# Optimization experiments

Measured on AMD Instinct MI355X. Metric: run time of the kernel, lower is better.

Reference implementation:

```python
import jax, jax.numpy as jnp
import numpy as np

E = 8        # num_experts
K = 2        # num_experts_per_tok
H = 1024     # hidden_dim
F = 2816     # intermediate_dim
R = 256      # shared-core rank
B, S = 2, 1024


def setup_inputs() -> dict:
    key = jax.random.key(0)
    ks = jax.random.split(key, 12)
    inp = {
        "hidden_states": jax.random.normal(ks[0], (B, S, H), jnp.float32),
        "gate_w": jax.random.normal(ks[1], (H, E), jnp.float32) / np.sqrt(H),
        # gate_proj: hidden -> intermediate, factored W_e = Ug[e] @ Cg @ Vg[e]
        "Ug": jax.random.normal(ks[2], (E, H, R), jnp.float32) / np.sqrt(H),
        "Cg": jax.random.normal(ks[3], (R, R), jnp.float32) / np.sqrt(R),
        "Vg": jax.random.normal(ks[4], (E, R, F), jnp.float32) / np.sqrt(R),
        # up_proj: hidden -> intermediate
        "Uu": jax.random.normal(ks[5], (E, H, R), jnp.float32) / np.sqrt(H),
        "Cu": jax.random.normal(ks[6], (R, R), jnp.float32) / np.sqrt(R),
        "Vu": jax.random.normal(ks[7], (E, R, F), jnp.float32) / np.sqrt(R),
        # down_proj: intermediate -> hidden
        "Ud": jax.random.normal(ks[8], (E, F, R), jnp.float32) / np.sqrt(F),
        "Cd": jax.random.normal(ks[9], (R, R), jnp.float32) / np.sqrt(R),
        "Vd": jax.random.normal(ks[10], (E, R, H), jnp.float32) / np.sqrt(R),
    }
    return inp


def _moe_forward(x, gate_w, Ug, Cg, Vg, Uu, Cu, Vu, Ud, Cd, Vd):
    b, s, h = x.shape
    xf = x.reshape(-1, h)                       # [T, H]
    T = xf.shape[0]
    logits = xf @ gate_w                        # [T, E]
    probs = jax.nn.softmax(logits, axis=-1)
    w, idx = jax.lax.top_k(probs, K)            # [T, K]
    w = w / jnp.sum(w, axis=-1, keepdims=True)
    # dense combine weights: combine[t, e] = sum of renormalized routing
    # weights over top-k slots routed to expert e (scatter-add in torch code)
    combine = jnp.zeros((T, E), xf.dtype).at[jnp.arange(T)[:, None], idx].add(w)
    out = jnp.zeros_like(xf)
    for e in range(E):  # fixed small expert count
        g = (xf @ Ug[e]) @ Cg @ Vg[e]           # [T, F]
        u = (xf @ Uu[e]) @ Cu @ Vu[e]           # [T, F]
        a = jax.nn.silu(g) * u
        y = (a @ Ud[e]) @ Cd @ Vd[e]            # [T, H]
        out = out + combine[:, e:e + 1] * y
    return out.reshape(b, s, h)


def reference(hidden_states, gate_w, Ug, Cg, Vg, Uu, Cu, Vu, Ud, Cd, Vd):
    return _moe_forward(hidden_states, gate_w, Ug, Cg, Vg, Uu, Cu, Vu, Ud, Cd, Vd)
```

## Files before the change

kernel.cpp:

```cpp
#include <hip/hip_runtime.h>
#include <math.h>

constexpr int cE = 8;
constexpr int cH = 1024;
constexpr int cF = 2816;
constexpr int cR = 256;
constexpr int cT = 2048;
constexpr int ROWS = cT * 2;
constexpr int LDA = 40;

using short8  = __attribute__((ext_vector_type(8))) short;
using float4v = __attribute__((ext_vector_type(4))) float;
#define MFMA16 __builtin_amdgcn_mfma_f32_16x16x32_bf16

__device__ __forceinline__ unsigned short f2bf(float f) {
  union { float f; unsigned u; } v; v.f = f;
  unsigned r = v.u + 0x7fffu + ((v.u >> 16) & 1u);
  return (unsigned short)(r >> 16);
}
__device__ __forceinline__ float bf2f(unsigned short s) {
  union { unsigned u; float f; } v; v.u = (unsigned)s << 16; return v.f;
}

__device__ __forceinline__ void store_bf8(unsigned short* dst, float4 a, float4 b) {
  union { unsigned short u[8]; uint4 v; } t;
  t.u[0] = f2bf(a.x); t.u[1] = f2bf(a.y); t.u[2] = f2bf(a.z); t.u[3] = f2bf(a.w);
  t.u[4] = f2bf(b.x); t.u[5] = f2bf(b.y); t.u[6] = f2bf(b.z); t.u[7] = f2bf(b.w);
  *reinterpret_cast<uint4*>(dst) = t.v;
}

__device__ __forceinline__ void gld16(const unsigned short* g, unsigned short* l) {
  __builtin_amdgcn_global_load_lds(
      (const __attribute__((address_space(1))) void*)g,
      (__attribute__((address_space(3))) void*)l, 16, 0, 0);
}

__device__ __forceinline__ void tconv_tile64(
    const float* __restrict__ in, unsigned short* __restrict__ out,
    int P, int Q, int e, int bx, int by, int tid, float (*tile)[65])
{
  const long es = (long)P * Q;
  in += e * es; out += e * es;
  const int c0 = bx * 64, r0 = by * 64;
  const int r = tid >> 4, c4 = (tid & 15) * 4;
#pragma unroll
  for (int p = 0; p < 4; ++p) {
    float4 v = *reinterpret_cast<const float4*>(
        in + (long)(r0 + p * 16 + r) * Q + c0 + c4);
    tile[p * 16 + r][c4 + 0] = v.x; tile[p * 16 + r][c4 + 1] = v.y;
    tile[p * 16 + r][c4 + 2] = v.z; tile[p * 16 + r][c4 + 3] = v.w;
  }
  __syncthreads();
  const int cc = tid >> 4, rr4 = (tid & 15) * 4;
#pragma unroll
  for (int p = 0; p < 4; ++p) {
    ushort4 o;
    o.x = f2bf(tile[rr4 + 0][p * 16 + cc]);
    o.y = f2bf(tile[rr4 + 1][p * 16 + cc]);
    o.z = f2bf(tile[rr4 + 2][p * 16 + cc]);
    o.w = f2bf(tile[rr4 + 3][p * 16 + cc]);
    *reinterpret_cast<ushort4*>(out + (long)(c0 + p * 16 + cc) * P + r0 + rr4) = o;
  }
}

constexpr int P1_TCONV = 544;
constexpr int PREP1_BLOCKS = P1_TCONV + cT / 4;

__global__ __launch_bounds__(256) void k_prep1s(
    const float* __restrict__ Cg, unsigned short* __restrict__ CgT,
    const float* __restrict__ Cu, unsigned short* __restrict__ CuT,
    const float* __restrict__ Vd, unsigned short* __restrict__ VdT,
    const float* __restrict__ x, const float* __restrict__ gw,
    unsigned short* __restrict__ xb, int* __restrict__ et,
    float* __restrict__ wt)
{
  __shared__ float tile[64][65];
  int b = blockIdx.x;
  const int tid = threadIdx.x;
  if (b < P1_TCONV) {
    const float* in; unsigned short* out; int P, Q;
    if (b < 16)       { in = Cg; out = CgT; P = 256; Q = 256;  }
    else if (b < 32)  { b -= 16; in = Cu; out = CuT; P = 256; Q = 256;  }
    else              { b -= 32; in = Vd; out = VdT; P = 256; Q = 1024; }
    const int tpe = (P / 64) * (Q / 64);
    const int e = b / tpe, rem = b % tpe;
    const int bx = rem % (Q / 64), by = rem / (Q / 64);
    tconv_tile64(in, out, P, Q, e, bx, by, tid, tile);
    return;
  }
  const int wid = tid >> 6, lane = tid & 63;
  const int t = (b - P1_TCONV) * 4 + wid;
  const float* xr = x + (long)t * cH + lane * 16;
  float4 v0 = *reinterpret_cast<const float4*>(xr);
  float4 v1 = *reinterpret_cast<const float4*>(xr + 4);
  float4 v2 = *reinterpret_cast<const float4*>(xr + 8);
  float4 v3 = *reinterpret_cast<const float4*>(xr + 12);
  store_bf8(xb + (long)t * cH + lane * 16, v0, v1);
  store_bf8(xb + (long)t * cH + lane * 16 + 8, v2, v3);
  float xv[16];
  *reinterpret_cast<float4*>(&xv[0])  = v0;
  *reinterpret_cast<float4*>(&xv[4])  = v1;
  *reinterpret_cast<float4*>(&xv[8])  = v2;
  *reinterpret_cast<float4*>(&xv[12]) = v3;
  const float* g = gw + (long)lane * 16 * cE;
  float l[cE];
#pragma unroll
  for (int e = 0; e < cE; ++e) l[e] = 0.f;
#pragma unroll
  for (int i = 0; i < 16; ++i) {
    float4 ga = *reinterpret_cast<const float4*>(g + i * cE);
    float4 gb = *reinterpret_cast<const float4*>(g + i * cE + 4);
    float xi = xv[i];
    l[0] += xi * ga.x; l[1] += xi * ga.y; l[2] += xi * ga.z; l[3] += xi * ga.w;
    l[4] += xi * gb.x; l[5] += xi * gb.y; l[6] += xi * gb.z; l[7] += xi * gb.w;
  }
#pragma unroll
  for (int m = 1; m < 64; m <<= 1)
#pragma unroll
    for (int e = 0; e < cE; ++e)
      l[e] += __shfl_xor(l[e], m, 64);
  if (lane == 0) {
    int i0 = 0; float m0 = l[0];
#pragma unroll
    for (int e = 1; e < cE; ++e) if (l[e] > m0) { m0 = l[e]; i0 = e; }
    int i1 = -1; float m1 = -1e30f;
#pragma unroll
    for (int e = 0; e < cE; ++e) if (e != i0 && l[e] > m1) { m1 = l[e]; i1 = e; }
    float w0 = 1.f / (1.f + expf(m1 - m0));
    et[t * 2 + 0] = i0;  et[t * 2 + 1] = i1;
    wt[t * 2 + 0] = w0;  wt[t * 2 + 1] = 1.f - w0;
  }
}

__device__ __forceinline__ void foldm_body(
    const unsigned short* __restrict__ A, const float* __restrict__ B,
    unsigned short* __restrict__ D, int ldd, int m0, int n0, int tid,
    unsigned short* As, unsigned short* Bs)
{
  const int sr = tid >> 2, sk = (tid & 3) * 8;
  const unsigned short* a0 = A + (long)(m0 + sr) * 256 + sk;
  const unsigned short* a1 = a0 + (long)64 * 256;
  const float* br = B + (long)(n0 + sr) * 256 + sk;
  uint4 rA0, rA1; float4 rB0, rB1;
  auto load_slice = [&](int k0) {
    rA0 = *reinterpret_cast<const uint4*>(a0 + k0);
    rA1 = *reinterpret_cast<const uint4*>(a1 + k0);
    rB0 = *reinterpret_cast<const float4*>(br + k0);
    rB1 = *reinterpret_cast<const float4*>(br + k0 + 4);
  };
  load_slice(0);
  const int wid = tid >> 6, lane = tid & 63;
  const int wm = (wid >> 1) * 64, wn = (wid & 1) * 32;
  const int fr = lane & 15, fq = lane >> 4;
  float4v zf = {0.f, 0.f, 0.f, 0.f};
  float4v acc[4][2];
#pragma unroll
  for (int i = 0; i < 4; ++i) { acc[i][0] = zf; acc[i][1] = zf; }
  for (int k0 = 0; k0 < 256; k0 += 32) {
    *reinterpret_cast<uint4*>(&As[sr * LDA + sk]) = rA0;
    *reinterpret_cast<uint4*>(&As[(sr + 64) * LDA + sk]) = rA1;
    store_bf8(&Bs[sr * LDA + sk], rB0, rB1);
    if (k0 + 32 < 256) load_slice(k0 + 32);
    __syncthreads();
    short8 af[4], bf[2];
#pragma unroll
    for (int mi = 0; mi < 4; ++mi)
      af[mi] = *reinterpret_cast<const short8*>(&As[(wm + mi * 16 + fr) * LDA + fq * 8]);
#pragma unroll
    for (int nj = 0; nj < 2; ++nj)
      bf[nj] = *reinterpret_cast<const short8*>(&Bs[(wn + nj * 16 + fr) * LDA + fq * 8]);
#pragma unroll
    for (int mi = 0; mi < 4; ++mi)
#pragma unroll
      for (int nj = 0; nj < 2; ++nj)
        acc[mi][nj] = MFMA16(af[mi], bf[nj], acc[mi][nj], 0, 0, 0);
    __syncthreads();
  }
#pragma unroll
  for (int mi = 0; mi < 4; ++mi)
#pragma unroll
    for (int r = 0; r < 4; ++r) {
      int m = m0 + wm + mi * 16 + fq * 4 + r;
#pragma unroll
      for (int nj = 0; nj < 2; ++nj)
        D[(long)m * ldd + n0 + wn + nj * 16 + fr] = f2bf(acc[mi][nj][r]);
    }
}

constexpr int PREP2_BLOCKS = 769 + 3 * 1408;
__global__ __launch_bounds__(256, 3) void k_prep2(
    const unsigned short* __restrict__ CgT, const unsigned short* __restrict__ CuT,
    const float* __restrict__ Ug, const float* __restrict__ Uu,
    unsigned short* __restrict__ b1t,
    const unsigned short* __restrict__ VdT, const float* __restrict__ Cd,
    unsigned short* __restrict__ vd2t,
    const float* __restrict__ Vg, unsigned short* __restrict__ vgT,
    const float* __restrict__ Vu, unsigned short* __restrict__ vuT,
    const float* __restrict__ Ud, unsigned short* __restrict__ udT,
    const int* __restrict__ et, int* __restrict__ rowmap,
    int* __restrict__ tok, int* __restrict__ cnt, int* __restrict__ off)
{
  __shared__ __align__(16) char smem[64 * 65 * 4];
  const int b = blockIdx.x;
  const int tid = threadIdx.x;
  if (b < 512) {
    unsigned short* As = (unsigned short*)smem;
    unsigned short* Bs = As + 128 * LDA;
    const int bx = b & 15, by = (b >> 4) & 1, z = b >> 5;
    const int sel = z >> 3, e = z & 7;
    const unsigned short* A = sel ? CuT : CgT;
    const float* B = (sel ? Uu : Ug) + (long)e * cH * cR;
    unsigned short* Dp = b1t + (long)e * 512 * 1024 + (long)sel * 256 * 1024;
    foldm_body(A, B, Dp, cH, by * 128, bx * 64, tid, As, Bs);
  } else if (b < 768) {
    unsigned short* As = (unsigned short*)smem;
    unsigned short* Bs = As + 128 * LDA;
    const int b2 = b - 512;
    const int bx = b2 & 3, by = (b2 >> 2) & 7, e = b2 >> 5;
    foldm_body(VdT + (long)e * cH * cR, Cd, vd2t + (long)e * cH * 256, cR,
               by * 128, bx * 64, tid, As, Bs);
  } else if (b == 768) {
    int* sc_ = (int*)smem;
    int* sp_ = sc_ + cE;
    int* so_ = sc_ + 2 * cE;
    if (tid < cE) { sc_[tid] = 0; sp_[tid] = 0; }
    __syncthreads();
    for (int i = tid; i < ROWS; i += 256) atomicAdd(&sc_[et[i]], 1);
    __syncthreads();
    if (tid == 0) {
      int s = 0;
      for (int e = 0; e < cE; ++e) { so_[e] = s; s += sc_[e]; }
    }
    __syncthreads();
    for (int i = tid; i < ROWS; i += 256) {
      int e = et[i];
      int slot = atomicAdd(&sp_[e], 1);
      int cr = so_[e] + slot;
      rowmap[i] = cr;
      tok[cr] = i >> 1;
    }
    if (tid < cE) { cnt[tid] = sc_[tid]; off[tid] = so_[tid]; }
  } else {
    float (*tile)[65] = reinterpret_cast<float(*)[65]>(smem);
    int t = b - 769;
    const float* in; unsigned short* out; int P, Q;
    if (t < 1408)       { in = Vg; out = vgT; P = 256;  Q = 2816; }
    else if (t < 2816)  { t -= 1408; in = Vu; out = vuT; P = 256;  Q = 2816; }
    else                { t -= 2816; in = Ud; out = udT; P = 2816; Q = 256;  }
    const int tpe = (P / 64) * (Q / 64);
    const int e = t / tpe, rem = t % tpe;
    const int bx = rem % (Q / 64), by = rem / (Q / 64);
    tconv_tile64(in, out, P, Q, e, bx, by, tid, tile);
  }
}

__global__ __launch_bounds__(256, 4) void k_t1c(
    const unsigned short* __restrict__ xb, const unsigned short* __restrict__ b1t,
    unsigned short* __restrict__ t1, const int* __restrict__ tok,
    const int* __restrict__ cnt, const int* __restrict__ off)
{
  __shared__ __align__(16) unsigned short As[2][64 * 64], Bs[2][64 * 64];
  const int e = blockIdx.z, c = cnt[e], o = off[e];
  const int m0 = blockIdx.y * 64;
  if (m0 >= c) return;
  const int n0 = blockIdx.x * 64;
  const int tid = threadIdx.x;
  const int wid = tid >> 6, lane = tid & 63;
  const int sr8 = lane >> 3;
  const int scs = ((lane & 7) ^ sr8) * 8;
  const unsigned short* gA[2];
#pragma unroll
  for (int j = 0; j < 2; ++j) {
    int row = min(m0 + wid * 16 + j * 8 + sr8, c - 1);
    gA[j] = xb + (long)tok[o + row] * cH + scs;
  }
  const unsigned short* gB = b1t + (long)e * 512 * 1024 +
      (long)(n0 + wid * 16 + sr8) * 1024 + scs;
  const int lofs = wid * 16 * 64;
  auto STAGE = [&](int k0, int buf) {
    gld16(gA[0] + k0, &As[buf][lofs]);
    gld16(gA[1] + k0, &As[buf][lofs + 8 * 64]);
    gld16(gB + k0, &Bs[buf][lofs]);
    gld16(gB + (long)8 * 1024 + k0, &Bs[buf][lofs + 8 * 64]);
  };
  const int wm = (wid >> 1) * 32, wn = (wid & 1) * 32;
  const int fr = lane & 15, fq = lane >> 4;
  const int swz = (fr & 7) * 8;
  float4v zf = {0.f, 0.f, 0.f, 0.f};
  float4v acc[2][2] = {{zf, zf}, {zf, zf}};
  STAGE(0, 0);
  __syncthreads();
  for (int t = 0; t < 16; ++t) {
    const int cur = t & 1;
    if (t < 15) STAGE((t + 1) * 64, cur ^ 1);
#pragma unroll
    for (int ks = 0; ks < 2; ++ks) {
      short8 af[2], bf[2];
#pragma unroll
      for (int mi = 0; mi < 2; ++mi)
        af[mi] = *reinterpret_cast<const short8*>(
            &As[cur][(wm + mi * 16 + fr) * 64 + ((ks * 32 + fq * 8) ^ swz)]);
#pragma unroll
      for (int nj = 0; nj < 2; ++nj)
        bf[nj] = *reinterpret_cast<const short8*>(
            &Bs[cur][(wn + nj * 16 + fr) * 64 + ((ks * 32 + fq * 8) ^ swz)]);
#pragma unroll
      for (int mi = 0; mi < 2; ++mi)
#pragma unroll
        for (int nj = 0; nj < 2; ++nj)
          acc[mi][nj] = MFMA16(af[mi], bf[nj], acc[mi][nj], 0, 0, 0);
    }
    __syncthreads();
  }
#pragma unroll
  for (int mi = 0; mi < 2; ++mi)
#pragma unroll
    for (int r = 0; r < 4; ++r) {
      int row = m0 + wm + mi * 16 + fq * 4 + r;
      if (row < c) {
#pragma unroll
        for (int nj = 0; nj < 2; ++nj)
          t1[(long)(o + row) * 512 + n0 + wn + nj * 16 + fr] = f2bf(acc[mi][nj][r]);
      }
    }
}

__global__ __launch_bounds__(256, 4) void k_act(
    const unsigned short* __restrict__ t1,
    const unsigned short* __restrict__ vgT, const unsigned short* __restrict__ vuT,
    unsigned short* __restrict__ a, const int* __restrict__ cnt,
    const int* __restrict__ off)
{
  __shared__ __align__(16) unsigned short Ag[2][64 * 32], Au[2][64 * 32];
  __shared__ __align__(16) unsigned short Bg[2][64 * 32], Bu[2][64 * 32];
  const int e = blockIdx.z, c = cnt[e], o = off[e];
  const int m0 = blockIdx.y * 64;
  if (m0 >= c) return;
  const int n0 = blockIdx.x * 64;
  const int tid = threadIdx.x;
  const int wid = tid >> 6, lane = tid & 63;
  const int sr16 = lane >> 2;
  const int scs = (((lane & 3) ^ (sr16 & 3)) * 8);
  const int ra = o + min(m0 + wid * 16 + sr16, c - 1);
  const unsigned short* gAg = t1 + (long)ra * 512 + scs;
  const unsigned short* gBg = vgT + (long)e * cF * 256 + (long)(n0 + wid * 16 + sr16) * 256 + scs;
  const unsigned short* gBu = vuT + (long)e * cF * 256 + (long)(n0 + wid * 16 + sr16) * 256 + scs;
  const int lofs = wid * 16 * 32;
  auto STAGE = [&](int k0, int buf) {
    gld16(gAg + k0, &Ag[buf][lofs]);
    gld16(gAg + 256 + k0, &Au[buf][lofs]);
    gld16(gBg + k0, &Bg[buf][lofs]);
    gld16(gBu + k0, &Bu[buf][lofs]);
  };
  const int wm = (wid >> 1) * 32, wn = (wid & 1) * 32;
  const int fr = lane & 15, fq = lane >> 4;
  const int swz = (fr & 3) * 8;
  float4v zf = {0.f, 0.f, 0.f, 0.f};
  float4v accg[2][2] = {{zf, zf}, {zf, zf}};
  float4v accu[2][2] = {{zf, zf}, {zf, zf}};
  STAGE(0, 0);
  __syncthreads();
  for (int t = 0; t < 8; ++t) {
    const int cur = t & 1;
    if (t < 7) STAGE((t + 1) * 32, cur ^ 1);
    short8 ag[2], au[2], bg[2], bu[2];
#pragma unroll
    for (int mi = 0; mi < 2; ++mi) {
      ag[mi] = *reinterpret_cast<const short8*>(
          &Ag[cur][(wm + mi * 16 + fr) * 32 + ((fq * 8) ^ swz)]);
      au[mi] = *reinterpret_cast<const short8*>(
          &Au[cur][(wm + mi * 16 + fr) * 32 + ((fq * 8) ^ swz)]);
    }
#pragma unroll
    for (int nj = 0; nj < 2; ++nj) {
      bg[nj] = *reinterpret_cast<const short8*>(
          &Bg[cur][(wn + nj * 16 + fr) * 32 + ((fq * 8) ^ swz)]);
      bu[nj] = *reinterpret_cast<const short8*>(
          &Bu[cur][(wn + nj * 16 + fr) * 32 + ((fq * 8) ^ swz)]);
    }
#pragma unroll
    for (int mi = 0; mi < 2; ++mi)
#pragma unroll
      for (int nj = 0; nj < 2; ++nj) {
        accg[mi][nj] = MFMA16(ag[mi], bg[nj], accg[mi][nj], 0, 0, 0);
        accu[mi][nj] = MFMA16(au[mi], bu[nj], accu[mi][nj], 0, 0, 0);
      }
    __syncthreads();
  }
#pragma unroll
  for (int mi = 0; mi < 2; ++mi)
#pragma unroll
    for (int r = 0; r < 4; ++r) {
      int row = m0 + wm + mi * 16 + fq * 4 + r;
      if (row < c) {
#pragma unroll
        for (int nj = 0; nj < 2; ++nj) {
          float g = accg[mi][nj][r];
          float u = accu[mi][nj][r];
          float s = g / (1.f + expf(-g)) * u;
          a[(long)(o + row) * cF + n0 + wn + nj * 16 + fr] = f2bf(s);
        }
      }
    }
}

__global__ __launch_bounds__(256, 4) void k_t3(
    const unsigned short* __restrict__ a, const unsigned short* __restrict__ udT,
    float* __restrict__ t3p, const int* __restrict__ cnt,
    const int* __restrict__ off)
{
  __shared__ __align__(16) unsigned short As[2][64 * 64], Bs[2][64 * 64];
  const int e = blockIdx.z, c = cnt[e], o = off[e];
  const int m0 = blockIdx.y * 64;
  if (m0 >= c) return;
  const int n0 = (blockIdx.x & 3) * 64;
  const int ksp = blockIdx.x >> 2;
  const int kbase = ksp * 704;
  const int tid = threadIdx.x;
  const int wid = tid >> 6, lane = tid & 63;
  const int sr8 = lane >> 3;
  const int scs = ((lane & 7) ^ sr8) * 8;
  const int ra0 = o + min(m0 + wid * 16 + sr8, c - 1);
  const int ra1 = o + min(m0 + wid * 16 + 8 + sr8, c - 1);
  const unsigned short* gA0 = a + (long)ra0 * cF + kbase + scs;
  const unsigned short* gA1 = a + (long)ra1 * cF + kbase + scs;
  const unsigned short* gB  = udT + (long)e * 256 * cF +
      (long)(n0 + wid * 16 + sr8) * cF + kbase + scs;
  const int lofs = wid * 16 * 64;
  auto STAGE = [&](int k0, int buf) {
    gld16(gA0 + k0, &As[buf][lofs]);
    gld16(gA1 + k0, &As[buf][lofs + 8 * 64]);
    gld16(gB + k0, &Bs[buf][lofs]);
    gld16(gB + (long)8 * cF + k0, &Bs[buf][lofs + 8 * 64]);
  };
  const int wm = (wid >> 1) * 32, wn = (wid & 1) * 32;
  const int fr = lane & 15, fq = lane >> 4;
  const int swz = (fr & 7) * 8;
  float4v zf = {0.f, 0.f, 0.f, 0.f};
  float4v acc[2][2] = {{zf, zf}, {zf, zf}};
  STAGE(0, 0);
  __syncthreads();
  for (int t = 0; t < 11; ++t) {
    const int cur = t & 1;
    if (t < 10) STAGE((t + 1) * 64, cur ^ 1);
#pragma unroll
    for (int ks = 0; ks < 2; ++ks) {
      short8 af[2], bf[2];
#pragma unroll
      for (int mi = 0; mi < 2; ++mi)
        af[mi] = *reinterpret_cast<const short8*>(
            &As[cur][(wm + mi * 16 + fr) * 64 + ((ks * 32 + fq * 8) ^ swz)]);
#pragma unroll
      for (int nj = 0; nj < 2; ++nj)
        bf[nj] = *reinterpret_cast<const short8*>(
            &Bs[cur][(wn + nj * 16 + fr) * 64 + ((ks * 32 + fq * 8) ^ swz)]);
#pragma unroll
      for (int mi = 0; mi < 2; ++mi)
#pragma unroll
        for (int nj = 0; nj < 2; ++nj)
          acc[mi][nj] = MFMA16(af[mi], bf[nj], acc[mi][nj], 0, 0, 0);
    }
    __syncthreads();
  }
  float* dstbase = t3p + (long)ksp * ROWS * 256;
#pragma unroll
  for (int mi = 0; mi < 2; ++mi)
#pragma unroll
    for (int r = 0; r < 4; ++r) {
      int row = m0 + wm + mi * 16 + fq * 4 + r;
      if (row < c) {
        float* dst = dstbase + (long)(o + row) * 256 + n0 + wn;
#pragma unroll
        for (int nj = 0; nj < 2; ++nj)
          dst[nj * 16 + fr] = acc[mi][nj][r];
      }
    }
}

__global__ __launch_bounds__(256) void k_red(
    const float* __restrict__ t3p, unsigned short* __restrict__ t3b)
{
  const long psz = (long)ROWS * 256;
  long i = ((long)blockIdx.x * 256 + threadIdx.x) * 8;
  float4 s0 = *reinterpret_cast<const float4*>(t3p + i);
  float4 s1 = *reinterpret_cast<const float4*>(t3p + i + 4);
#pragma unroll
  for (int q = 1; q < 4; ++q) {
    float4 a0 = *reinterpret_cast<const float4*>(t3p + q * psz + i);
    float4 a1 = *reinterpret_cast<const float4*>(t3p + q * psz + i + 4);
    s0.x += a0.x; s0.y += a0.y; s0.z += a0.z; s0.w += a0.w;
    s1.x += a1.x; s1.y += a1.y; s1.z += a1.z; s1.w += a1.w;
  }
  store_bf8(t3b + i, s0, s1);
}

__global__ __launch_bounds__(256, 4) void k_y(
    const unsigned short* __restrict__ t3b, const unsigned short* __restrict__ vd2t,
    unsigned short* __restrict__ y, const int* __restrict__ cnt,
    const int* __restrict__ off)
{
  __shared__ __align__(16) unsigned short As[2][64 * 32], Bs[2][64 * 32];
  const int e = blockIdx.z, c = cnt[e], o = off[e];
  const int m0 = blockIdx.y * 64;
  if (m0 >= c) return;
  const int n0 = blockIdx.x * 64;
  const int tid = threadIdx.x;
  const int wid = tid >> 6, lane = tid & 63;
  const int sr16 = lane >> 2;
  const int scs = (((lane & 3) ^ (sr16 & 3)) * 8);
  const int ra = o + min(m0 + wid * 16 + sr16, c - 1);
  const unsigned short* gA = t3b + (long)ra * 256 + scs;
  const unsigned short* gB = vd2t + (long)e * cH * 256 + (long)(n0 + wid * 16 + sr16) * 256 + scs;
  const int lofs = wid * 16 * 32;
  auto STAGE = [&](int k0, int buf) {
    gld16(gA + k0, &As[buf][lofs]);
    gld16(gB + k0, &Bs[buf][lofs]);
  };
  const int wm = (wid >> 1) * 32, wn = (wid & 1) * 32;
  const int fr = lane & 15, fq = lane >> 4;
  const int swz = (fr & 3) * 8;
  float4v zf = {0.f, 0.f, 0.f, 0.f};
  float4v acc[2][2] = {{zf, zf}, {zf, zf}};
  STAGE(0, 0);
  __syncthreads();
  for (int t = 0; t < 8; ++t) {
    const int cur = t & 1;
    if (t < 7) STAGE((t + 1) * 32, cur ^ 1);
    short8 af[2], bf[2];
#pragma unroll
    for (int mi = 0; mi < 2; ++mi)
      af[mi] = *reinterpret_cast<const short8*>(
          &As[cur][(wm + mi * 16 + fr) * 32 + ((fq * 8) ^ swz)]);
#pragma unroll
    for (int nj = 0; nj < 2; ++nj)
      bf[nj] = *reinterpret_cast<const short8*>(
          &Bs[cur][(wn + nj * 16 + fr) * 32 + ((fq * 8) ^ swz)]);
#pragma unroll
    for (int mi = 0; mi < 2; ++mi)
#pragma unroll
      for (int nj = 0; nj < 2; ++nj)
        acc[mi][nj] = MFMA16(af[mi], bf[nj], acc[mi][nj], 0, 0, 0);
    __syncthreads();
  }
#pragma unroll
  for (int mi = 0; mi < 2; ++mi)
#pragma unroll
    for (int r = 0; r < 4; ++r) {
      int row = m0 + wm + mi * 16 + fq * 4 + r;
      if (row < c) {
#pragma unroll
        for (int nj = 0; nj < 2; ++nj)
          y[(long)(o + row) * cH + n0 + wn + nj * 16 + fr] = f2bf(acc[mi][nj][r]);
      }
    }
}

__global__ __launch_bounds__(256) void k_combine(
    const unsigned short* __restrict__ y, const float* __restrict__ wt,
    const int* __restrict__ rowmap, float* __restrict__ out)
{
  const int tid = threadIdx.x;
  const int t = blockIdx.x * 2 + (tid >> 7);
  const int h = (tid & 127) * 8;
  const int r0 = rowmap[2 * t], r1 = rowmap[2 * t + 1];
  const float w0 = wt[2 * t], w1 = wt[2 * t + 1];
  union { uint4 v; unsigned short s[8]; } ua, ub;
  ua.v = *reinterpret_cast<const uint4*>(y + (long)r0 * cH + h);
  ub.v = *reinterpret_cast<const uint4*>(y + (long)r1 * cH + h);
  float o[8];
#pragma unroll
  for (int i = 0; i < 8; ++i)
    o[i] = w0 * bf2f(ua.s[i]) + w1 * bf2f(ub.s[i]);
  float* dst = out + (long)t * cH + h;
  *reinterpret_cast<float4*>(dst)     = make_float4(o[0], o[1], o[2], o[3]);
  *reinterpret_cast<float4*>(dst + 4) = make_float4(o[4], o[5], o[6], o[7]);
}

extern "C" void kernel_launch(void* const* d_in, const int* in_sizes, int n_in,
                              void* d_out, int out_size, void* d_ws, size_t ws_size,
                              hipStream_t stream)
{
  const float* x  = (const float*)d_in[0];
  const float* gw = (const float*)d_in[1];
  const float* Ug = (const float*)d_in[2];
  const float* Cg = (const float*)d_in[3];
  const float* Vg = (const float*)d_in[4];
  const float* Uu = (const float*)d_in[5];
  const float* Cu = (const float*)d_in[6];
  const float* Vu = (const float*)d_in[7];
  const float* Ud = (const float*)d_in[8];
  const float* Cd = (const float*)d_in[9];
  const float* Vd = (const float*)d_in[10];
  float* out = (float*)d_out;

  char* w = (char*)d_ws;
  unsigned short* vgT = (unsigned short*)w;
  float*          t3p = (float*)w;
  unsigned short* t3b = (unsigned short*)(w + (long)4 * ROWS * 256 * 4);
  w += (long)cE * cF * 256 * 2;
  unsigned short* b1t = (unsigned short*)w;  w += (long)cE * 512 * 1024 * 2;
  unsigned short* vd2t = (unsigned short*)w; w += (long)cE * cH * 256 * 2;
  unsigned short* vuT = (unsigned short*)w;
  unsigned short* yb  = (unsigned short*)w;  w += (long)cE * cF * 256 * 2;
  unsigned short* udT = (unsigned short*)w;  w += (long)cE * 256 * cF * 2;
  unsigned short* VdT = (unsigned short*)w;  w += (long)cE * cH * 256 * 2;
  unsigned short* xb  = (unsigned short*)w;  w += (long)cT * cH * 2;
  unsigned short* CgT = (unsigned short*)w;  w += (long)cR * cR * 2;
  unsigned short* CuT = (unsigned short*)w;  w += (long)cR * cR * 2;
  unsigned short* t1  = (unsigned short*)w;  w += (long)ROWS * 512 * 2;
  unsigned short* ab  = (unsigned short*)w;  w += (long)ROWS * cF * 2;
  float* wt   = (float*)w; w += ROWS * 4;
  int* et     = (int*)w; w += ROWS * 4;
  int* rowmap = (int*)w; w += ROWS * 4;
  int* tok    = (int*)w; w += ROWS * 4;
  int* cnt = (int*)w; w += cE * 4;
  int* off = (int*)w; w += cE * 4;

  k_prep1s<<<dim3(PREP1_BLOCKS), dim3(256), 0, stream>>>(
      Cg, CgT, Cu, CuT, Vd, VdT, x, gw, xb, et, wt);
  k_prep2<<<dim3(PREP2_BLOCKS), dim3(256), 0, stream>>>(
      CgT, CuT, Ug, Uu, b1t, VdT, Cd, vd2t,
      Vg, vgT, Vu, vuT, Ud, udT, et, rowmap, tok, cnt, off);
  k_t1c<<<dim3(8, cT / 64, cE), dim3(256), 0, stream>>>(xb, b1t, t1, tok, cnt, off);
  k_act<<<dim3(cF / 64, cT / 64, cE), dim3(256), 0, stream>>>(t1, vgT, vuT, ab, cnt, off);
  k_t3<<<dim3(16, cT / 64, cE), dim3(256), 0, stream>>>(ab, udT, t3p, cnt, off);
  k_red<<<dim3(ROWS * 256 / (256 * 8)), dim3(256), 0, stream>>>(t3p, t3b);
  k_y<<<dim3(cH / 64, cT / 64, cE), dim3(256), 0, stream>>>(t3b, vd2t, yb, cnt, off);
  k_combine<<<dim3(cT / 2), dim3(256), 0, stream>>>(yb, wt, rowmap, out);
}
```

Before: 259.5 us.

## Give each wave private LDS tiles in k_act to drop block barriers

The k_act fused gate/up GEMM now has each wave load its own A and B fragments into a private LDS region instead of sharing cooperatively loaded tiles. All __syncthreads calls are replaced with per-wave s_waitcnt vmcnt waits, double-buffered with eight outstanding loads. This removes block-wide barrier stalls but doubles global/LDS traffic, since A and B rows are now loaded redundantly across waves. LDS usage grows to 64KB per block, and launch bounds drop to 2 blocks per CU.

New measurement: 261.9 us. Within noise of the previous version (+0.9%).

```diff
diff --git a/kernel.cpp b/kernel.cpp
--- a/kernel.cpp
+++ b/kernel.cpp
@@ -34,6 +34,11 @@
       (const __attribute__((address_space(1))) void*)g,
       (__attribute__((address_space(3))) void*)l, 16, 0, 0);
 }
+
+#define VMWAIT8() do { asm volatile("s_waitcnt vmcnt(8)" ::: "memory"); \
+                       __builtin_amdgcn_sched_barrier(0); } while (0)
+#define VMWAIT0() do { asm volatile("s_waitcnt vmcnt(0)" ::: "memory"); \
+                       __builtin_amdgcn_sched_barrier(0); } while (0)
 
 __device__ __forceinline__ void tconv_tile64(
     const float* __restrict__ in, unsigned short* __restrict__ out,
@@ -325,58 +330,69 @@
     }
 }
 
-__global__ __launch_bounds__(256, 4) void k_act(
+__global__ __launch_bounds__(256, 2) void k_act(
     const unsigned short* __restrict__ t1,
     const unsigned short* __restrict__ vgT, const unsigned short* __restrict__ vuT,
     unsigned short* __restrict__ a, const int* __restrict__ cnt,
     const int* __restrict__ off)
 {
-  __shared__ __align__(16) unsigned short Ag[2][64 * 32], Au[2][64 * 32];
-  __shared__ __align__(16) unsigned short Bg[2][64 * 32], Bu[2][64 * 32];
+  __shared__ __align__(16) unsigned short S[4][2][4096];
   const int e = blockIdx.z, c = cnt[e], o = off[e];
   const int m0 = blockIdx.y * 64;
   if (m0 >= c) return;
   const int n0 = blockIdx.x * 64;
   const int tid = threadIdx.x;
   const int wid = tid >> 6, lane = tid & 63;
-  const int sr16 = lane >> 2;
-  const int scs = (((lane & 3) ^ (sr16 & 3)) * 8);
-  const int ra = o + min(m0 + wid * 16 + sr16, c - 1);
-  const unsigned short* gAg = t1 + (long)ra * 512 + scs;
-  const unsigned short* gBg = vgT + (long)e * cF * 256 + (long)(n0 + wid * 16 + sr16) * 256 + scs;
-  const unsigned short* gBu = vuT + (long)e * cF * 256 + (long)(n0 + wid * 16 + sr16) * 256 + scs;
-  const int lofs = wid * 16 * 32;
+  const int wm = (wid >> 1) * 32, wn = (wid & 1) * 32;
+  const int sr = lane >> 2;
+  const int scs = (((lane & 3) ^ (sr & 3)) * 8);
+  const int ra0 = o + min(m0 + wm + sr, c - 1);
+  const int ra1 = o + min(m0 + wm + 16 + sr, c - 1);
+  const unsigned short* gA0 = t1 + (long)ra0 * 512 + scs;
+  const unsigned short* gA1 = t1 + (long)ra1 * 512 + scs;
+  const unsigned short* gBg0 = vgT + (long)e * cF * 256 +
+      (long)(n0 + wn + sr) * 256 + scs;
+  const unsigned short* gBg1 = gBg0 + 16 * 256;
+  const unsigned short* gBu0 = vuT + (long)e * cF * 256 +
+      (long)(n0 + wn + sr) * 256 + scs;
+  const unsigned short* gBu1 = gBu0 + 16 * 256;
+  unsigned short* Sw = &S[wid][0][0];
   auto STAGE = [&](int k0, int buf) {
-    gld16(gAg + k0, &Ag[buf][lofs]);
-    gld16(gAg + 256 + k0, &Au[buf][lofs]);
-    gld16(gBg + k0, &Bg[buf][lofs]);
-    gld16(gBu + k0, &Bu[buf][lofs]);
+    unsigned short* B = Sw + buf * 4096;
+    gld16(gA0 + k0,        B);
+    gld16(gA1 + k0,        B + 16 * 32);
+    gld16(gA0 + 256 + k0,  B + 1024);
+    gld16(gA1 + 256 + k0,  B + 1024 + 16 * 32);
+    gld16(gBg0 + k0,       B + 2048);
+    gld16(gBg1 + k0,       B + 2048 + 16 * 32);
+    gld16(gBu0 + k0,       B + 3072);
+    gld16(gBu1 + k0,       B + 3072 + 16 * 32);
   };
-  const int wm = (wid >> 1) * 32, wn = (wid & 1) * 32;
   const int fr = lane & 15, fq = lane >> 4;
   const int swz = (fr & 3) * 8;
   float4v zf = {0.f, 0.f, 0.f, 0.f};
   float4v accg[2][2] = {{zf, zf}, {zf, zf}};
   float4v accu[2][2] = {{zf, zf}, {zf, zf}};
   STAGE(0, 0);
-  __syncthreads();
   for (int t = 0; t < 8; ++t) {
     const int cur = t & 1;
-    if (t < 7) STAGE((t + 1) * 32, cur ^ 1);
+    if (t < 7) { STAGE((t + 1) * 32, cur ^ 1); VMWAIT8(); }
+    else       { VMWAIT0(); }
+    const unsigned short* B = Sw + cur * 4096;
     short8 ag[2], au[2], bg[2], bu[2];
 #pragma unroll
     for (int mi = 0; mi < 2; ++mi) {
       ag[mi] = *reinterpret_cast<const short8*>(
-          &Ag[cur][(wm + mi * 16 + fr) * 32 + ((fq * 8) ^ swz)]);
+          &B[(mi * 16 + fr) * 32 + ((fq * 8) ^ swz)]);
       au[mi] = *reinterpret_cast<const short8*>(
-          &Au[cur][(wm + mi * 16 + fr) * 32 + ((fq * 8) ^ swz)]);
+          &B[1024 + (mi * 16 + fr) * 32 + ((fq * 8) ^ swz)]);
     }
 #pragma unroll
     for (int nj = 0; nj < 2; ++nj) {
       bg[nj] = *reinterpret_cast<const short8*>(
-          &Bg[cur][(wn + nj * 16 + fr) * 32 + ((fq * 8) ^ swz)]);
+          &B[2048 + (nj * 16 + fr) * 32 + ((fq * 8) ^ swz)]);
       bu[nj] = *reinterpret_cast<const short8*>(
-          &Bu[cur][(wn + nj * 16 + fr) * 32 + ((fq * 8) ^ swz)]);
+          &B[3072 + (nj * 16 + fr) * 32 + ((fq * 8) ^ swz)]);
     }
 #pragma unroll
     for (int mi = 0; mi < 2; ++mi)
@@ -385,7 +401,6 @@
         accg[mi][nj] = MFMA16(ag[mi], bg[nj], accg[mi][nj], 0, 0, 0);
         accu[mi][nj] = MFMA16(au[mi], bu[nj], accu[mi][nj], 0, 0, 0);
       }
-    __syncthreads();
   }
 #pragma unroll
   for (int mi = 0; mi < 2; ++mi)
```
